# Optimization experiments

Hardware: AMD Instinct MI355X
Metric: run time of the kernel (lower is better)

Reference implementation:

```python
import jax, jax.numpy as jnp
import numpy as np

LN_EPS = 1e-5  # torch LayerNorm default


def _seg_mean(table, neigh_idx, num_seg):
    """Gather neighbor rows then unsorted-segment-mean (fixed fan-out S)."""
    S = neigh_idx.shape[0] // num_seg
    gathered = table[neigh_idx]  # [B*S, D] irregular gather
    seg = jnp.repeat(jnp.arange(num_seg), S)
    summed = jax.ops.segment_sum(gathered, seg, num_segments=num_seg)
    return summed / jnp.asarray(S, dtype=table.dtype)


def _block(agg, self_feats, W, b, gamma, beta):
    # concat -> Linear -> ReLU -> LayerNorm (dropout is identity in eval)
    h = jnp.concatenate([agg, self_feats], axis=-1) @ W + b
    h = jax.nn.relu(h)
    mu = jnp.mean(h, axis=-1, keepdims=True)
    var = jnp.mean((h - mu) ** 2, axis=-1, keepdims=True)
    return gamma * (h - mu) * jax.lax.rsqrt(var + LN_EPS) + beta


def setup_inputs() -> dict:
    key = jax.random.key(0)
    ks = jax.random.split(key, 10)
    N, D, H1, H2 = 100000, 256, 256, 256
    B, S1, S2 = 16384, 10, 10
    feats = jax.random.normal(ks[0], (N, D), dtype=jnp.float32)
    hidden1 = jax.random.uniform(ks[1], (N, H1), dtype=jnp.float32)  # torch.rand init
    hidden2 = jax.random.uniform(ks[2], (N, H2), dtype=jnp.float32)
    node_batch = jax.random.randint(ks[3], (B,), 0, N)
    neigh1 = jax.random.randint(ks[4], (B * S1,), 0, N)
    neigh2 = jax.random.randint(ks[5], (B * S2,), 0, N)
    W1 = jax.random.normal(ks[6], (2 * D, H1), dtype=jnp.float32) * 0.05
    W2 = jax.random.normal(ks[7], (2 * H1, H2), dtype=jnp.float32) * 0.05
    return {
        "feats": feats, "hidden1": hidden1, "hidden2": hidden2,
        "W1": W1, "b1": jnp.zeros((H1,)), "g1": jnp.ones((H1,)), "be1": jnp.zeros((H1,)),
        "W2": W2, "b2": jnp.zeros((H2,)), "g2": jnp.ones((H2,)), "be2": jnp.zeros((H2,)),
        "node_batch": node_batch, "neigh1": neigh1, "neigh2": neigh2,
    }


def reference(feats, hidden1, hidden2, W1, b1, g1, be1, W2, b2, g2, be2,
              node_batch, neigh1, neigh2):
    B = node_batch.shape[0]
    # layer 1: aggregate raw features (hidden['layer 0'])
    agg1 = _seg_mean(feats, neigh1, B)
    h1 = _block(agg1, feats[node_batch], W1, b1, g1, be1)  # [B, H1]
    # layer 2: aggregate from the OLD hidden1 table (original updates tables
    # only after the loop finishes)
    agg2 = _seg_mean(hidden1, neigh2, B)
    h2 = _block(agg2, hidden1[node_batch], W2, b2, g2, be2)  # [B, H2]
    new_hidden2 = hidden2.at[node_batch].set(h2)
    return h2, new_hidden2
```

## Files before the change

### kernel.cpp

```cpp
#include <hip/hip_runtime.h>

#define HDIM 256
#define KDIM 512
#define ROWS 16
#define XBPAD 8
#define LN_EPS 1e-5f

typedef __attribute__((ext_vector_type(8))) short bf16x8;
typedef __attribute__((ext_vector_type(4))) float f32x4;

static __device__ __forceinline__ unsigned short f2bf(float f) {
    union { float f; unsigned u; } v; v.f = f;
    unsigned r = v.u + 0x7FFF + ((v.u >> 16) & 1);
    return (unsigned short)(r >> 16);
}

__global__ __launch_bounds__(256) void prep_w2(
    const float* __restrict__ W2, unsigned short* __restrict__ W2f)
{
    int tid = blockIdx.x * 256 + threadIdx.x;
    if (tid >= 16 * 16 * 64) return;
    int l  = tid & 63;
    int ks = (tid >> 6) & 15;
    int ct = tid >> 10;
    int col = ct * 16 + (l & 15);
    int k0  = ks * 32 + (l >> 4) * 8;
    unsigned short pk[8];
    #pragma unroll
    for (int j = 0; j < 8; ++j)
        pk[j] = f2bf(W2[(size_t)(k0 + j) * HDIM + col]);
    *(uint4*)&W2f[(size_t)tid * 8] = *(uint4*)pk;
}

__global__ __launch_bounds__(256) void copy_init_kernel(
    const float4* __restrict__ src, float4* __restrict__ dst,
    int* __restrict__ winner, const int* __restrict__ node_batch,
    int n4, int B)
{
    int tid = blockIdx.x * blockDim.x + threadIdx.x;
    int stride = gridDim.x * blockDim.x;
    for (int i = tid; i < n4; i += stride) dst[i] = src[i];
    for (int i = tid; i < B; i += stride) winner[node_batch[i]] = -1;
}

__global__ __launch_bounds__(256) void winner_kernel(
    int* __restrict__ winner, const int* __restrict__ node_batch, int B)
{
    int i = blockIdx.x * blockDim.x + threadIdx.x;
    if (i < B) atomicMax(&winner[node_batch[i]], i);
}

template <int SC>
__global__ __launch_bounds__(512, 4) void mfma_kernel(
    const float* __restrict__ hidden1,
    const unsigned short* __restrict__ W2f,
    const int* __restrict__ node_batch,
    const int* __restrict__ neigh2,
    float* __restrict__ hout,
    int B, int S_rt)
{
    __shared__ unsigned short xbf[ROWS][KDIM + XBPAD];
    const int t    = threadIdx.x;
    const int lane = t & 63;
    const int w    = t >> 6;
    const int row0 = blockIdx.x * ROWS;

    #pragma unroll
    for (int rr = 0; rr < 2; ++rr) {
        const int r = w + rr * 8;
        int b = row0 + r;
        if (b >= B) b = B - 1;
        const int selfidx = node_batch[b];
        float4 a = make_float4(0.f, 0.f, 0.f, 0.f);
        if constexpr (SC > 0) {
            const int* nb = neigh2 + (size_t)b * SC;
            int idx[SC > 0 ? SC : 1];
            #pragma unroll
            for (int s = 0; s < SC; ++s) idx[s] = nb[s];
            #pragma unroll
            for (int s = 0; s < SC; ++s) {
                float4 v = *(const float4*)&hidden1[(size_t)idx[s] * HDIM + 4 * lane];
                a.x += v.x; a.y += v.y; a.z += v.z; a.w += v.w;
            }
            const float invS = 1.0f / (float)SC;
            a.x *= invS; a.y *= invS; a.z *= invS; a.w *= invS;
        } else {
            const int* nb = neigh2 + (size_t)b * S_rt;
            for (int s = 0; s < S_rt; ++s) {
                float4 v = *(const float4*)&hidden1[(size_t)nb[s] * HDIM + 4 * lane];
                a.x += v.x; a.y += v.y; a.z += v.z; a.w += v.w;
            }
            const float invS = 1.0f / (float)S_rt;
            a.x *= invS; a.y *= invS; a.z *= invS; a.w *= invS;
        }
        float4 sv = *(const float4*)&hidden1[(size_t)selfidx * HDIM + 4 * lane];
        unsigned short pa[4] = { f2bf(a.x), f2bf(a.y), f2bf(a.z), f2bf(a.w) };
        unsigned short ps[4] = { f2bf(sv.x), f2bf(sv.y), f2bf(sv.z), f2bf(sv.w) };
        *(uint2*)&xbf[r][4 * lane]        = *(uint2*)pa;
        *(uint2*)&xbf[r][HDIM + 4 * lane] = *(uint2*)ps;
    }
    __syncthreads();

    const int arow = lane & 15;
    const int g8   = (lane >> 4) * 8;
    f32x4 acc0 = {0.f, 0.f, 0.f, 0.f};
    f32x4 acc1 = {0.f, 0.f, 0.f, 0.f};
    const unsigned short* bp0 = W2f + ((size_t)(2 * w) * 1024 + lane) * 8;
    const unsigned short* bp1 = W2f + ((size_t)(2 * w + 1) * 1024 + lane) * 8;

    #pragma unroll
    for (int ks = 0; ks < 16; ++ks) {
        bf16x8 af = *(const bf16x8*)&xbf[arow][ks * 32 + g8];
        bf16x8 b0 = *(const bf16x8*)(bp0 + ks * 512);
        bf16x8 b1 = *(const bf16x8*)(bp1 + ks * 512);
        acc0 = __builtin_amdgcn_mfma_f32_16x16x32_bf16(af, b0, acc0, 0, 0, 0);
        acc1 = __builtin_amdgcn_mfma_f32_16x16x32_bf16(af, b1, acc1, 0, 0, 0);
    }

    #pragma unroll
    for (int p = 0; p < 4; ++p) {
        const int drow = (lane >> 4) * 4 + p;
        const size_t rbase = (size_t)(row0 + drow) * HDIM;
        hout[rbase + 2 * w * 16 + (lane & 15)]       = acc0[p];
        hout[rbase + (2 * w + 1) * 16 + (lane & 15)] = acc1[p];
    }
}

__global__ __launch_bounds__(256) void ln_kernel(
    float* __restrict__ out_h2,
    float* __restrict__ out_tab,
    const float* __restrict__ bias2,
    const float* __restrict__ gamma2,
    const float* __restrict__ beta2,
    const int* __restrict__ node_batch,
    const int* __restrict__ winner,
    int B)
{
    const int lane = threadIdx.x & 63;
    const int row  = blockIdx.x * 4 + (threadIdx.x >> 6);
    if (row >= B) return;

    float4 hv = *(const float4*)&out_h2[(size_t)row * HDIM + 4 * lane];
    float4 bb = *(const float4*)&bias2[4 * lane];
    float4 gg = *(const float4*)&gamma2[4 * lane];
    float4 ee = *(const float4*)&beta2[4 * lane];
    float bbar[4] = {bb.x, bb.y, bb.z, bb.w};
    float gar[4]  = {gg.x, gg.y, gg.z, gg.w};
    float ear[4]  = {ee.x, ee.y, ee.z, ee.w};

    float v[4];
    float s = 0.f, q = 0.f;
    {
        float hh[4] = {hv.x, hv.y, hv.z, hv.w};
        #pragma unroll
        for (int jj = 0; jj < 4; ++jj) {
            float h = fmaxf(hh[jj] + bbar[jj], 0.0f);
            v[jj] = h;
            s += h;
            q += h * h;
        }
    }
    #pragma unroll
    for (int off = 32; off > 0; off >>= 1) {
        s += __shfl_xor(s, off, 64);
        q += __shfl_xor(q, off, 64);
    }
    float mu   = s * (1.0f / (float)HDIM);
    float var  = q * (1.0f / (float)HDIM) - mu * mu;
    float rstd = rsqrtf(var + LN_EPS);

    float4 o;
    o.x = gar[0] * (v[0] - mu) * rstd + ear[0];
    o.y = gar[1] * (v[1] - mu) * rstd + ear[1];
    o.z = gar[2] * (v[2] - mu) * rstd + ear[2];
    o.w = gar[3] * (v[3] - mu) * rstd + ear[3];
    *(float4*)&out_h2[(size_t)row * HDIM + 4 * lane] = o;
    int node = node_batch[row];
    if (winner[node] == row)
        *(float4*)&out_tab[(size_t)node * HDIM + 4 * lane] = o;
}

extern "C" void kernel_launch(void* const* d_in, const int* in_sizes, int n_in,
                              void* d_out, int out_size, void* d_ws, size_t ws_size,
                              hipStream_t stream) {
    const float* hidden1 = (const float*)d_in[1];
    const float* hidden2 = (const float*)d_in[2];
    const float* W2      = (const float*)d_in[7];
    const float* b2      = (const float*)d_in[8];
    const float* g2      = (const float*)d_in[9];
    const float* be2     = (const float*)d_in[10];
    const int* node_batch = (const int*)d_in[11];
    const int* neigh2     = (const int*)d_in[13];

    const int B  = in_sizes[11];
    const int S  = in_sizes[13] / B;
    const int NH = in_sizes[2];

    float* out_h2  = (float*)d_out;
    float* out_tab = out_h2 + (size_t)B * HDIM;
    int* winner = (int*)d_ws;
    unsigned short* W2f = (unsigned short*)((char*)d_ws + 512 * 1024);

    hipLaunchKernelGGL(prep_w2, dim3(64), dim3(256), 0, stream, W2, W2f);
    hipLaunchKernelGGL(copy_init_kernel, dim3(2048), dim3(256), 0, stream,
                       (const float4*)hidden2, (float4*)out_tab,
                       winner, node_batch, NH / 4, B);
    hipLaunchKernelGGL(winner_kernel, dim3((B + 255) / 256), dim3(256), 0, stream,
                       winner, node_batch, B);
    dim3 grid((B + ROWS - 1) / ROWS);
    if (S == 10) {
        hipLaunchKernelGGL((mfma_kernel<10>), grid, dim3(512), 0, stream,
                           hidden1, W2f, node_batch, neigh2, out_h2, B, S);
    } else {
        hipLaunchKernelGGL((mfma_kernel<0>), grid, dim3(512), 0, stream,
                           hidden1, W2f, node_batch, neigh2, out_h2, B, S);
    }
    hipLaunchKernelGGL(ln_kernel, dim3((B + 3) / 4), dim3(256), 0, stream,
                       out_h2, out_tab, b2, g2, be2, node_batch, winner, B);
}
```

Before: 91.08 us.

## Fuse table copy and winner atomics into MFMA kernel via interleaved blocks

Even-indexed blocks of the main kernel now copy the hidden2 table into the output and run the winner atomicMax, while odd-indexed blocks do the gather plus MFMA GEMM. The winner reset moves into the W2 prep kernel, cutting the launch count from five to three. The aim is to overlap the bandwidth-bound table copy with the gather/GEMM work and remove launch gaps between the small kernels. In exchange, both kinds of work compete for bandwidth and CU slots, and the grid sizing assumes the copy-block count and row-block count line up.

After: 88.28 us. 1.03x faster.

```diff
diff --git a/kernel.cpp b/kernel.cpp
--- a/kernel.cpp
+++ b/kernel.cpp
@@ -5,6 +5,7 @@
 #define ROWS 16
 #define XBPAD 8
 #define LN_EPS 1e-5f
+#define COPY_BLOCKS 1024
 
 typedef __attribute__((ext_vector_type(8))) short bf16x8;
 typedef __attribute__((ext_vector_type(4))) float f32x4;
@@ -15,10 +16,12 @@
     return (unsigned short)(r >> 16);
 }
 
-__global__ __launch_bounds__(256) void prep_w2(
-    const float* __restrict__ W2, unsigned short* __restrict__ W2f)
+__global__ __launch_bounds__(256) void prep_init_kernel(
+    const float* __restrict__ W2, unsigned short* __restrict__ W2f,
+    int* __restrict__ winner, const int* __restrict__ node_batch, int B)
 {
     int tid = blockIdx.x * 256 + threadIdx.x;
+    for (int i = tid; i < B; i += 64 * 256) winner[node_batch[i]] = -1;
     if (tid >= 16 * 16 * 64) return;
     int l  = tid & 63;
     int ks = (tid >> 6) & 15;
@@ -32,38 +35,32 @@
     *(uint4*)&W2f[(size_t)tid * 8] = *(uint4*)pk;
 }
 
-__global__ __launch_bounds__(256) void copy_init_kernel(
-    const float4* __restrict__ src, float4* __restrict__ dst,
-    int* __restrict__ winner, const int* __restrict__ node_batch,
-    int n4, int B)
-{
-    int tid = blockIdx.x * blockDim.x + threadIdx.x;
-    int stride = gridDim.x * blockDim.x;
-    for (int i = tid; i < n4; i += stride) dst[i] = src[i];
-    for (int i = tid; i < B; i += stride) winner[node_batch[i]] = -1;
-}
-
-__global__ __launch_bounds__(256) void winner_kernel(
-    int* __restrict__ winner, const int* __restrict__ node_batch, int B)
-{
-    int i = blockIdx.x * blockDim.x + threadIdx.x;
-    if (i < B) atomicMax(&winner[node_batch[i]], i);
-}
-
 template <int SC>
-__global__ __launch_bounds__(512, 4) void mfma_kernel(
+__global__ __launch_bounds__(512, 4) void fused_kernel(
     const float* __restrict__ hidden1,
+    const float4* __restrict__ h2src,
     const unsigned short* __restrict__ W2f,
     const int* __restrict__ node_batch,
     const int* __restrict__ neigh2,
+    int* __restrict__ winner,
     float* __restrict__ hout,
-    int B, int S_rt)
+    float* __restrict__ out_tab,
+    int n4, int B, int S_rt)
 {
+    if ((blockIdx.x & 1) == 0) {
+        const int tid = (blockIdx.x >> 1) * 512 + threadIdx.x;
+        const int stride = COPY_BLOCKS * 512;
+        float4* dst = (float4*)out_tab;
+        for (int i = tid; i < n4; i += stride) dst[i] = h2src[i];
+        for (int i = tid; i < B; i += stride) atomicMax(&winner[node_batch[i]], i);
+        return;
+    }
+
     __shared__ unsigned short xbf[ROWS][KDIM + XBPAD];
     const int t    = threadIdx.x;
     const int lane = t & 63;
     const int w    = t >> 6;
-    const int row0 = blockIdx.x * ROWS;
+    const int row0 = (blockIdx.x >> 1) * ROWS;
 
     #pragma unroll
     for (int rr = 0; rr < 2; ++rr) {
@@ -201,19 +198,21 @@
     int* winner = (int*)d_ws;
     unsigned short* W2f = (unsigned short*)((char*)d_ws + 512 * 1024);
 
-    hipLaunchKernelGGL(prep_w2, dim3(64), dim3(256), 0, stream, W2, W2f);
-    hipLaunchKernelGGL(copy_init_kernel, dim3(2048), dim3(256), 0, stream,
-                       (const float4*)hidden2, (float4*)out_tab,
-                       winner, node_batch, NH / 4, B);
-    hipLaunchKernelGGL(winner_kernel, dim3((B + 255) / 256), dim3(256), 0, stream,
-                       winner, node_batch, B);
-    dim3 grid((B + ROWS - 1) / ROWS);
+    hipLaunchKernelGGL(prep_init_kernel, dim3(64), dim3(256), 0, stream,
+                       W2, W2f, winner, node_batch, B);
+
+    const int mfma_blocks = (B + ROWS - 1) / ROWS;
+    dim3 grid(2 * ((COPY_BLOCKS > mfma_blocks) ? COPY_BLOCKS : mfma_blocks));
     if (S == 10) {
-        hipLaunchKernelGGL((mfma_kernel<10>), grid, dim3(512), 0, stream,
-                           hidden1, W2f, node_batch, neigh2, out_h2, B, S);
+        hipLaunchKernelGGL((fused_kernel<10>), grid, dim3(512), 0, stream,
+                           hidden1, (const float4*)hidden2, W2f,
+                           node_batch, neigh2, winner, out_h2, out_tab,
+                           NH / 4, B, S);
     } else {
-        hipLaunchKernelGGL((mfma_kernel<0>), grid, dim3(512), 0, stream,
-                           hidden1, W2f, node_batch, neigh2, out_h2, B, S);
+        hipLaunchKernelGGL((fused_kernel<0>), grid, dim3(512), 0, stream,
+                           hidden1, (const float4*)hidden2, W2f,
+                           node_batch, neigh2, winner, out_h2, out_tab,
+                           NH / 4, B, S);
     }
     hipLaunchKernelGGL(ln_kernel, dim3((B + 3) / 4), dim3(256), 0, stream,
                        out_h2, out_tab, b2, g2, be2, node_batch, winner, B);
```
